# Kernel tuning notes

Measured on AMD Instinct MI355X. Metric: run time of the kernel, lower is better.

The kernel has to match this reference:

```python
import jax, jax.numpy as jnp
import numpy as np

NUM_EMBEDDINGS = 8192
EMBED_DIM = 256
BETA = 0.25  # commitment loss weight (self.beta in the torch module)


def setup_inputs() -> dict:
    key = jax.random.key(0)
    k1, k2 = jax.random.split(key)
    z = jax.random.normal(k1, (16, EMBED_DIM, 32, 32), dtype=jnp.float32)
    # learned codebook (nn.Embedding weight), default init ~ N(0,1); scale for realism
    codebook = jax.random.normal(k2, (NUM_EMBEDDINGS, EMBED_DIM), dtype=jnp.float32)
    return {"z": z, "codebook": codebook}


def reference(z, codebook):
    # channel_last: [B, C, H, W] -> [B, H, W, C]
    zl = jnp.transpose(z, (0, 2, 3, 1))
    # d = ||e||^2 - 2 z.e  (the ||z||^2 term is constant w.r.t. argmin, as in source)
    d = jnp.sum(codebook * codebook, axis=1) - 2.0 * jnp.einsum('bhwd,nd->bhwn', zl, codebook)
    index = jnp.argmin(d, axis=-1)          # [B, H, W] int
    z_q = codebook[index]                   # [B, H, W, C]
    loss = (jnp.mean((jax.lax.stop_gradient(z_q) - zl) ** 2)
            + BETA * jnp.mean((z_q - jax.lax.stop_gradient(zl)) ** 2))
    # straight-through estimator
    z_q_st = zl + jax.lax.stop_gradient(z_q - zl)
    # diversity: mean over batch of (#unique codes used per sample) / (#positions per sample)
    B = index.shape[0]
    flat = index.reshape(B, -1)             # [B, HW]
    presence = jnp.zeros((B, NUM_EMBEDDINGS), jnp.float32).at[
        jnp.arange(B)[:, None], flat].set(1.0)
    diversity = presence.sum() / jnp.float32(flat.size)
    # channel_first: [B, H, W, C] -> [B, C, H, W]
    z_q_out = jnp.transpose(z_q_st, (0, 3, 1, 2))
    return z_q_out, index, loss, diversity
```

## Files before the change

### kernel.cpp

```cpp
#include <hip/hip_runtime.h>
#include <cstdint>

typedef unsigned short u16;
typedef unsigned int   u32;
typedef __attribute__((ext_vector_type(8))) short bf16x8;
typedef __attribute__((ext_vector_type(4))) float f32x4;

#define NPOS    16384
#define DIM     256
#define NCODES  8192
#define ZSTRIDE 262144
#define NELEM   4194304
#define TAU     6e-3f
#define RCH     32


#define WS_AHI    0u
#define WS_ALO    8388608u
#define WS_BHI    16777216u
#define WS_BLO    20971520u
#define WS_E2     25165824u
#define WS_WV1    25198592u
#define WS_WI1    25722880u
#define WS_WV2    26247168u
#define WS_IDX    26771456u
#define WS_PRES   26836992u
#define WS_RCNT   26853376u
#define WS_LDEL   26853380u
#define WS_RLIST  26853632u
#define WS_PART   26919168u
#define WS_RBV    26920448u
#define WS_RBI    29017600u

__device__ __forceinline__ u16 f2bf(float x) {
    u32 u = __float_as_uint(x);
    return (u16)((u + 0x7FFFu + ((u >> 16) & 1u)) >> 16);
}
__device__ __forceinline__ float bf2f(u16 h) { return __uint_as_float((u32)h << 16); }

__device__ __forceinline__ void gload_lds16(const void* g, void* l) {
    __builtin_amdgcn_global_load_lds(
        (const __attribute__((address_space(1))) void*)g,
        (__attribute__((address_space(3))) void*)l, 16, 0, 0);
}

__device__ __forceinline__ void top2_push(float& v1, int& i1, float& v2, float d, int c) {
    const bool better = d < v1;
    v2 = fminf(v2, fmaxf(d, v1));
    v1 = fminf(v1, d);
    if (better) i1 = c;
}
__device__ __forceinline__ void top2_merge(float& v1, int& i1, float& v2,
                                           float ov1, int oi1, float ov2) {
    const bool better = ov1 < v1;
    v2 = fminf(fminf(v2, ov2), fmaxf(v1, ov1));
    v1 = fminf(v1, ov1);
    if (better) i1 = oi1;
}

__global__ __launch_bounds__(256)
void preprocess(const float* __restrict__ cb, const float* __restrict__ z,
                u16* __restrict__ Bhi, u16* __restrict__ Blo,
                u16* __restrict__ Ahi, u16* __restrict__ Alo,
                float* __restrict__ e2, u32* __restrict__ presence,
                int* __restrict__ rcnt, float* __restrict__ ldel) {
    __shared__ u16 his[128 * 34], los[128 * 34];
    const int bid = blockIdx.x;
    const int t   = threadIdx.x;

    if (bid < 2048) {
        if (bid < 16) presence[bid * 256 + t] = 0u;
        if (bid == 16 && t == 0) { rcnt[0] = 0; ldel[0] = 0.0f; }

        const int row  = bid * 4 + (t >> 6);
        const int lane = t & 63;
        const float4 v = *(const float4*)(cb + (size_t)row * DIM + lane * 4);
        float s = v.x * v.x + v.y * v.y + v.z * v.z + v.w * v.w;
#pragma unroll
        for (int o = 32; o > 0; o >>= 1) s += __shfl_xor(s, o);
        if (lane == 0) e2[row] = s;

        const float vv[4] = {v.x, v.y, v.z, v.w};
        u16 h[4], l[4];
#pragma unroll
        for (int j = 0; j < 4; ++j) { h[j] = f2bf(vv[j]); l[j] = f2bf(vv[j] - bf2f(h[j])); }

        const int nt = row >> 7, pr = row & 127, kt = lane >> 3;
        const int q  = (lane & 7) >> 1, off = (lane & 1) * 4;
        const int sw = (pr >> 1) & 3;
        const size_t dst = ((size_t)(nt * 8 + kt) * 128 + pr) * 32 + ((q ^ sw) << 3) + off;
        *(uint2*)(Bhi + dst) = make_uint2((u32)h[0] | ((u32)h[1] << 16), (u32)h[2] | ((u32)h[3] << 16));
        *(uint2*)(Blo + dst) = make_uint2((u32)l[0] | ((u32)l[1] << 16), (u32)l[2] | ((u32)l[3] << 16));
        return;
    }

    const int zb = bid - 2048;
    const int m = zb >> 3, kt = zb & 7;
    const int b = m >> 3, hw0 = (m & 7) * 128;
    const int p = t & 127, ch = t >> 7;

#pragma unroll
    for (int sub = 0; sub < 16; ++sub) {
        const int cl = sub * 2 + ch;
        const float v = z[(size_t)b * ZSTRIDE + (size_t)(kt * 32 + cl) * 1024 + hw0 + p];
        const u16 h = f2bf(v);
        his[p * 34 + cl] = h;
        los[p * 34 + cl] = f2bf(v - bf2f(h));
    }
    __syncthreads();
    const int p2 = t >> 1, c0 = (t & 1) * 2;
    const int sw = (p2 >> 1) & 3;
    const size_t base = ((size_t)(m * 8 + kt) * 128 + p2) * 32;
    u32 wh[8], wl[8];
    const int half = c0 * 8;
#pragma unroll
    for (int j = 0; j < 8; ++j) {
        wh[j] = (u32)his[p2 * 34 + half + 2 * j] | ((u32)his[p2 * 34 + half + 2 * j + 1] << 16);
        wl[j] = (u32)los[p2 * 34 + half + 2 * j] | ((u32)los[p2 * 34 + half + 2 * j + 1] << 16);
    }
    *(uint4*)(Ahi + base + (((c0 + 0) ^ sw) << 3)) = make_uint4(wh[0], wh[1], wh[2], wh[3]);
    *(uint4*)(Ahi + base + (((c0 + 1) ^ sw) << 3)) = make_uint4(wh[4], wh[5], wh[6], wh[7]);
    *(uint4*)(Alo + base + (((c0 + 0) ^ sw) << 3)) = make_uint4(wl[0], wl[1], wl[2], wl[3]);
    *(uint4*)(Alo + base + (((c0 + 1) ^ sw) << 3)) = make_uint4(wl[4], wl[5], wl[6], wl[7]);
}

__global__ __launch_bounds__(256, 2)
void gemm_argmin(const u16* __restrict__ Ahi, const u16* __restrict__ Alo,
                 const u16* __restrict__ Bhi, const u16* __restrict__ Blo,
                 const float* __restrict__ e2,
                 float* __restrict__ wv1, int* __restrict__ wi1, float* __restrict__ wv2) {
    __shared__ u16 sbuf[2][4][4096];
    __shared__ float lv1[256]; __shared__ int li1[256]; __shared__ float lv2[256];

    const int bid = blockIdx.x;
    const int ng  = bid & 7;
    const int mt  = bid >> 3;

    const int tid  = threadIdx.x;
    const int lane = tid & 63;
    const int wvi  = tid >> 6;
    const int wr   = wvi >> 1, wc = wvi & 1;
    const int l15  = lane & 15, lq = lane >> 4;
    const int woff = (tid & 192) * 16;
    const int src  = tid * 8;
    const int sel  = (l15 >> 1) & 3;
    const int ka   = ((lq ^ sel) << 3);

#define FRAG(base, row) (*(const bf16x8*)((base) + (row) * 32 + ka))
#define STAGE(bq, ss_) do {                                                     \
        const int nt_ = ng * 8 + ((ss_) >> 3), kt_ = (ss_) & 7;                 \
        const u16* Ah_ = Ahi + (size_t)(mt * 8 + kt_) * 4096;                   \
        const u16* Al_ = Alo + (size_t)(mt * 8 + kt_) * 4096;                   \
        const u16* Bh_ = Bhi + (size_t)(nt_ * 8 + kt_) * 4096;                  \
        const u16* Bl_ = Blo + (size_t)(nt_ * 8 + kt_) * 4096;                  \
        gload_lds16(Ah_ + src,        (char*)&sbuf[bq][0][0] + woff);           \
        gload_lds16(Ah_ + 2048 + src, (char*)&sbuf[bq][0][0] + 4096 + woff);    \
        gload_lds16(Al_ + src,        (char*)&sbuf[bq][1][0] + woff);           \
        gload_lds16(Al_ + 2048 + src, (char*)&sbuf[bq][1][0] + 4096 + woff);    \
        gload_lds16(Bh_ + src,        (char*)&sbuf[bq][2][0] + woff);           \
        gload_lds16(Bh_ + 2048 + src, (char*)&sbuf[bq][2][0] + 4096 + woff);    \
        gload_lds16(Bl_ + src,        (char*)&sbuf[bq][3][0] + woff);           \
        gload_lds16(Bl_ + 2048 + src, (char*)&sbuf[bq][3][0] + 4096 + woff);    \
    } while (0)

    float rv1[16], rv2[16]; int ri1[16];
#pragma unroll
    for (int e = 0; e < 16; ++e) { rv1[e] = 3e38f; rv2[e] = 3e38f; ri1[e] = 0; }

    f32x4 acc[4][4] = {};
    float e2v[4];
    int cbase = 0;

    STAGE(0, 0);
    __syncthreads();

    for (int ss = 0; ss < 64; ++ss) {
        const int cur = ss & 1;
        if (ss < 63) STAGE(cur ^ 1, ss + 1);

        if ((ss & 7) == 0) {
            const int nt = ng * 8 + (ss >> 3);
            cbase = nt * 128 + wc * 64 + l15;
#pragma unroll
            for (int ni = 0; ni < 4; ++ni) e2v[ni] = e2[cbase + ni * 16];
        }

        const u16* Ah = &sbuf[cur][0][0];
        const u16* Al = &sbuf[cur][1][0];
        const u16* Bh = &sbuf[cur][2][0];
        const u16* Bl = &sbuf[cur][3][0];

        bf16x8 ah[4], bh[4], xx[4];
#pragma unroll
        for (int i = 0; i < 4; ++i) ah[i] = FRAG(Ah, wr * 64 + i * 16 + l15);
#pragma unroll
        for (int i = 0; i < 4; ++i) bh[i] = FRAG(Bh, wc * 64 + i * 16 + l15);
#pragma unroll
        for (int i = 0; i < 4; ++i)
#pragma unroll
            for (int j = 0; j < 4; ++j)
                acc[i][j] = __builtin_amdgcn_mfma_f32_16x16x32_bf16(ah[i], bh[j], acc[i][j], 0, 0, 0);
#pragma unroll
        for (int i = 0; i < 4; ++i) xx[i] = FRAG(Bl, wc * 64 + i * 16 + l15);
#pragma unroll
        for (int i = 0; i < 4; ++i)
#pragma unroll
            for (int j = 0; j < 4; ++j)
                acc[i][j] = __builtin_amdgcn_mfma_f32_16x16x32_bf16(ah[i], xx[j], acc[i][j], 0, 0, 0);
#pragma unroll
        for (int i = 0; i < 4; ++i) xx[i] = FRAG(Al, wr * 64 + i * 16 + l15);
#pragma unroll
        for (int i = 0; i < 4; ++i)
#pragma unroll
            for (int j = 0; j < 4; ++j)
                acc[i][j] = __builtin_amdgcn_mfma_f32_16x16x32_bf16(xx[i], bh[j], acc[i][j], 0, 0, 0);

        if ((ss & 7) == 7) {
#pragma unroll
            for (int mi = 0; mi < 4; ++mi)
#pragma unroll
                for (int j = 0; j < 4; ++j) {
                    const int e = mi * 4 + j;
#pragma unroll
                    for (int ni = 0; ni < 4; ++ni) {
                        const float d = fmaf(-2.0f, acc[mi][ni][j], e2v[ni]);
                        top2_push(rv1[e], ri1[e], rv2[e], d, cbase + ni * 16);
                    }
                }
#pragma unroll
            for (int mi = 0; mi < 4; ++mi)
#pragma unroll
                for (int ni = 0; ni < 4; ++ni)
                    acc[mi][ni] = f32x4{0.f, 0.f, 0.f, 0.f};
        }
        __syncthreads();
    }

#pragma unroll
    for (int mi = 0; mi < 4; ++mi)
#pragma unroll
        for (int j = 0; j < 4; ++j) {
            const int e = mi * 4 + j;
            float v1 = rv1[e], v2 = rv2[e]; int i1 = ri1[e];
#pragma unroll
            for (int off = 1; off <= 8; off <<= 1) {
                const float ov1 = __shfl_xor(v1, off);
                const int   oi1 = __shfl_xor(i1, off);
                const float ov2 = __shfl_xor(v2, off);
                top2_merge(v1, i1, v2, ov1, oi1, ov2);
            }
            if (l15 == 0) {
                const int row = wr * 64 + mi * 16 + lq * 4 + j;
                lv1[row * 2 + wc] = v1; li1[row * 2 + wc] = i1; lv2[row * 2 + wc] = v2;
            }
        }
    __syncthreads();
    if (tid < 128) {
        float v1 = lv1[tid * 2], v2 = lv2[tid * 2]; int i1 = li1[tid * 2];
        top2_merge(v1, i1, v2, lv1[tid * 2 + 1], li1[tid * 2 + 1], lv2[tid * 2 + 1]);
        const size_t o = (size_t)ng * NPOS + (size_t)mt * 128 + tid;
        wv1[o] = v1; wi1[o] = i1; wv2[o] = v2;
    }
#undef FRAG
#undef STAGE
}

__global__ __launch_bounds__(256)
void merge_output(const float* __restrict__ wv1, const int* __restrict__ wi1,
                  const float* __restrict__ wv2,
                  const float* __restrict__ z, const float* __restrict__ cb,
                  float* __restrict__ out, float* __restrict__ out_idxf,
                  float* __restrict__ partial, u32* __restrict__ presence,
                  int* __restrict__ rcnt, int* __restrict__ rlist,
                  int* __restrict__ ws_idx) {
    __shared__ int codes[64];
    __shared__ float red[256];
    const int tile = blockIdx.x;
    const int b    = tile >> 4;
    const int hw0  = (tile & 15) * 64;
    const int tid  = threadIdx.x;
    const int m    = tid & 63;
    const int cg   = tid >> 6;

    if (cg == 0) {
        const int pos = tile * 64 + m;
        float v1 = 3e38f, v2 = 3e38f; int i1 = 0;
#pragma unroll
        for (int g = 0; g < 8; ++g) {
            const size_t o = (size_t)g * NPOS + pos;
            top2_merge(v1, i1, v2, wv1[o], wi1[o], wv2[o]);
        }
        codes[m]      = i1;
        ws_idx[pos]   = i1;
        out_idxf[pos] = (float)i1;
        if (v2 - v1 < TAU) {
            const int s = atomicAdd(rcnt, 1);
            rlist[s] = pos;
        } else {
            atomicOr(&presence[b * 256 + (i1 >> 5)], 1u << (i1 & 31));
        }
    }
    __syncthreads();

    const int code = codes[m];
    const float* crow = cb  + (size_t)code * DIM;
    const float* zb   = z   + (size_t)b * ZSTRIDE + hw0 + m;
    float*       ob   = out + (size_t)b * ZSTRIDE + hw0 + m;

    float lsum = 0.0f;
#pragma unroll
    for (int q = 0; q < 16; ++q) {
        const int c = (cg * 16 + q) * 4;
        const float4 e = *(const float4*)(crow + c);
        const float z0 = zb[(size_t)(c + 0) * 1024];
        const float z1 = zb[(size_t)(c + 1) * 1024];
        const float z2 = zb[(size_t)(c + 2) * 1024];
        const float z3 = zb[(size_t)(c + 3) * 1024];
        const float d0 = e.x - z0, d1 = e.y - z1, d2 = e.z - z2, d3 = e.w - z3;
        lsum += d0 * d0 + d1 * d1 + d2 * d2 + d3 * d3;
        ob[(size_t)(c + 0) * 1024] = z0 + d0;
        ob[(size_t)(c + 1) * 1024] = z1 + d1;
        ob[(size_t)(c + 2) * 1024] = z2 + d2;
        ob[(size_t)(c + 3) * 1024] = z3 + d3;
    }
    red[tid] = lsum;
    __syncthreads();
    for (int o = 128; o > 0; o >>= 1) {
        if (tid < o) red[tid] += red[tid + o];
        __syncthreads();
    }
    if (tid == 0) partial[tile] = red[0];
}

__global__ __launch_bounds__(256)
void rescue_scan(const float* __restrict__ z, const float* __restrict__ cb,
                 const float* __restrict__ e2, const int* __restrict__ rcnt,
                 const int* __restrict__ rlist,
                 float* __restrict__ rbv, int* __restrict__ rbi) {
    __shared__ float zvec[256];
    __shared__ float sv[256]; __shared__ int si[256];
    const int n = rcnt[0];
    const int t = threadIdx.x;
    for (int idx = blockIdx.x; idx < n * RCH; idx += gridDim.x) {
        const int e  = idx >> 5;
        const int ch = idx & 31;
        const int pos = rlist[e];
        const int b = pos >> 10, hw = pos & 1023;
        __syncthreads();
        zvec[t] = z[(size_t)b * ZSTRIDE + (size_t)t * 1024 + hw];
        __syncthreads();

        const int c = ch * 256 + t;
        const float* cr = cb + (size_t)c * DIM;
        float a0 = 0.f, a1 = 0.f, a2 = 0.f, a3 = 0.f;
#pragma unroll
        for (int k = 0; k < DIM; k += 16) {
            const float4 v0 = *(const float4*)(cr + k);
            const float4 v1 = *(const float4*)(cr + k + 4);
            const float4 v2 = *(const float4*)(cr + k + 8);
            const float4 v3 = *(const float4*)(cr + k + 12);
            a0 = fmaf(zvec[k + 0], v0.x, a0); a0 = fmaf(zvec[k + 1], v0.y, a0);
            a0 = fmaf(zvec[k + 2], v0.z, a0); a0 = fmaf(zvec[k + 3], v0.w, a0);
            a1 = fmaf(zvec[k + 4], v1.x, a1); a1 = fmaf(zvec[k + 5], v1.y, a1);
            a1 = fmaf(zvec[k + 6], v1.z, a1); a1 = fmaf(zvec[k + 7], v1.w, a1);
            a2 = fmaf(zvec[k + 8], v2.x, a2); a2 = fmaf(zvec[k + 9], v2.y, a2);
            a2 = fmaf(zvec[k +10], v2.z, a2); a2 = fmaf(zvec[k +11], v2.w, a2);
            a3 = fmaf(zvec[k +12], v3.x, a3); a3 = fmaf(zvec[k +13], v3.y, a3);
            a3 = fmaf(zvec[k +14], v3.z, a3); a3 = fmaf(zvec[k +15], v3.w, a3);
        }
        const float dot = (a0 + a1) + (a2 + a3);
        sv[t] = fmaf(-2.f, dot, e2[c]); si[t] = c;
        __syncthreads();
        for (int o = 128; o > 0; o >>= 1) {
            if (t < o) {
                const float ov = sv[t + o]; const int oi = si[t + o];
                if (ov < sv[t] || (ov == sv[t] && oi < si[t])) { sv[t] = ov; si[t] = oi; }
            }
            __syncthreads();
        }
        if (t == 0) { rbv[e * RCH + ch] = sv[0]; rbi[e * RCH + ch] = si[0]; }
    }
}

__global__ __launch_bounds__(256)
void rescue_fix(const float* __restrict__ z, const float* __restrict__ cb,
                const int* __restrict__ rcnt, const int* __restrict__ rlist,
                const float* __restrict__ rbv, const int* __restrict__ rbi,
                const int* __restrict__ ws_idx,
                float* __restrict__ out_idxf, u32* __restrict__ presence,
                float* __restrict__ out, float* __restrict__ ldel) {
    __shared__ int   bestc;
    __shared__ float red[4];
    const int n = rcnt[0];
    const int t = threadIdx.x;
    for (int e = blockIdx.x; e < n; e += gridDim.x) {
        const int pos = rlist[e];
        const int b = pos >> 10, hw = pos & 1023;
        if (t == 0) {
            float bv = 3e38f; int bi = 0x7fffffff;
            for (int ch = 0; ch < RCH; ++ch) {
                const float v = rbv[e * RCH + ch]; const int i = rbi[e * RCH + ch];
                if (v < bv || (v == bv && i < bi)) { bv = v; bi = i; }
            }
            bestc = bi;
            out_idxf[pos] = (float)bi;
            atomicOr(&presence[b * 256 + (bi >> 5)], 1u << (bi & 31));
        }
        __syncthreads();
        const int best = bestc;
        const int old  = ws_idx[pos];
        if (best != old) {
            const float zv = z[(size_t)b * ZSTRIDE + (size_t)t * 1024 + hw];
            const float en = cb[(size_t)best * DIM + t];
            const float eo = cb[(size_t)old  * DIM + t];
            const float dn = en - zv, dold = eo - zv;
            out[(size_t)b * ZSTRIDE + (size_t)t * 1024 + hw] = zv + dn;
            float dl = dn * dn - dold * dold;
#pragma unroll
            for (int o = 32; o > 0; o >>= 1) dl += __shfl_xor(dl, o);
            if ((t & 63) == 0) red[t >> 6] = dl;
            __syncthreads();
            if (t == 0) atomicAdd(ldel, red[0] + red[1] + red[2] + red[3]);
        }
        __syncthreads();
    }
}

__global__ __launch_bounds__(256)
void finalize_kernel(const float* __restrict__ partial,
                     const u32* __restrict__ presence,
                     const float* __restrict__ ldel,
                     float* __restrict__ out_loss, float* __restrict__ out_div) {
    __shared__ float sred[256];
    __shared__ int   ired[256];
    const int tid = threadIdx.x;
    float s = partial[tid];
    int cnt = 0;
    for (int w = tid; w < 16 * 256; w += 256) cnt += __popc(presence[w]);
    sred[tid] = s; ired[tid] = cnt;
    __syncthreads();
    for (int o = 128; o > 0; o >>= 1) {
        if (tid < o) { sred[tid] += sred[tid + o]; ired[tid] += ired[tid + o]; }
        __syncthreads();
    }
    if (tid == 0) {
        out_loss[0] = 1.25f * (sred[0] + ldel[0]) / (float)NELEM;
        out_div[0]  = (float)ired[0] / (float)NPOS;
    }
}

extern "C" void kernel_launch(void* const* d_in, const int* in_sizes, int n_in,
                              void* d_out, int out_size, void* d_ws, size_t ws_size,
                              hipStream_t stream) {
    const float* z  = (const float*)d_in[0];
    const float* cb = (const float*)d_in[1];
    float* out = (float*)d_out;
    char*  ws  = (char*)d_ws;

    u16*   Ahi = (u16*)(ws + WS_AHI);
    u16*   Alo = (u16*)(ws + WS_ALO);
    u16*   Bhi = (u16*)(ws + WS_BHI);
    u16*   Blo = (u16*)(ws + WS_BLO);
    float* e2  = (float*)(ws + WS_E2);
    float* wv1 = (float*)(ws + WS_WV1);
    int*   wi1 = (int*)(ws + WS_WI1);
    float* wv2 = (float*)(ws + WS_WV2);
    int*   ws_idx = (int*)(ws + WS_IDX);
    u32*   presence = (u32*)(ws + WS_PRES);
    int*   rcnt  = (int*)(ws + WS_RCNT);
    float* ldel  = (float*)(ws + WS_LDEL);
    int*   rlist = (int*)(ws + WS_RLIST);
    float* partial = (float*)(ws + WS_PART);
    float* rbv = (float*)(ws + WS_RBV);
    int*   rbi = (int*)(ws + WS_RBI);

    float* out_zq   = out;
    float* out_idxf = out + NELEM;
    float* out_loss = out + NELEM + NPOS;
    float* out_div  = out + NELEM + NPOS + 1;

    preprocess<<<3072, 256, 0, stream>>>(cb, z, Bhi, Blo, Ahi, Alo, e2, presence, rcnt, ldel);
    gemm_argmin<<<1024, 256, 0, stream>>>(Ahi, Alo, Bhi, Blo, e2, wv1, wi1, wv2);
    merge_output<<<NPOS / 64, 256, 0, stream>>>(wv1, wi1, wv2, z, cb, out_zq, out_idxf,
                                                partial, presence, rcnt, rlist, ws_idx);
    rescue_scan<<<2048, 256, 0, stream>>>(z, cb, e2, rcnt, rlist, rbv, rbi);
    rescue_fix<<<256, 256, 0, stream>>>(z, cb, rcnt, rlist, rbv, rbi, ws_idx,
                                        out_idxf, presence, out_zq, ldel);
    finalize_kernel<<<1, 256, 0, stream>>>(partial, presence, ldel, out_loss, out_div);
}
```

Measured before the change: 256.5 us.

## Cache e2 in LDS, relax GEMM barriers, warp-level reductions in rescue kernels

The GEMM kernel now copies its slice of codebook norms into shared memory once per block. Its per-step __syncthreads is replaced by an explicit vmcnt wait plus a raw s_barrier, so the prefetch of the next stage can stay in flight while the current one is consumed. The rescue scan gives each wave four codes per thread and reduces with wave shuffles instead of an LDS tree reduction with many block barriers. The rescue fix merges its 32 chunk results with a wave shuffle and launches more blocks. The hand-written waitcnt depends on the exact count of outstanding loads and could cause races if the compiler schedules differently.

```diff
diff --git a/kernel.cpp b/kernel.cpp
--- a/kernel.cpp
+++ b/kernel.cpp
@@ -130,6 +130,7 @@
                  const float* __restrict__ e2,
                  float* __restrict__ wv1, int* __restrict__ wi1, float* __restrict__ wv2) {
     __shared__ u16 sbuf[2][4][4096];
+    __shared__ __align__(16) float e2s[1024];
     __shared__ float lv1[256]; __shared__ int li1[256]; __shared__ float lv2[256];
 
     const int bid = blockIdx.x;
@@ -171,18 +172,27 @@
     float e2v[4];
     int cbase = 0;
 
+    reinterpret_cast<float4*>(e2s)[tid] = ((const float4*)e2)[ng * 256 + tid];
+    __syncthreads();
     STAGE(0, 0);
-    __syncthreads();
 
     for (int ss = 0; ss < 64; ++ss) {
         const int cur = ss & 1;
-        if (ss < 63) STAGE(cur ^ 1, ss + 1);
+        if (ss < 63) {
+            STAGE(cur ^ 1, ss + 1);
+            asm volatile("s_waitcnt vmcnt(8)" ::: "memory");
+        } else {
+            asm volatile("s_waitcnt vmcnt(0)" ::: "memory");
+        }
+        __builtin_amdgcn_s_barrier();
+        __builtin_amdgcn_sched_barrier(0);
 
         if ((ss & 7) == 0) {
-            const int nt = ng * 8 + (ss >> 3);
-            cbase = nt * 128 + wc * 64 + l15;
-#pragma unroll
-            for (int ni = 0; ni < 4; ++ni) e2v[ni] = e2[cbase + ni * 16];
+            const int ntl = ss >> 3;
+            cbase = (ng * 8 + ntl) * 128 + wc * 64 + l15;
+            const int eb = ntl * 128 + wc * 64 + l15;
+#pragma unroll
+            for (int ni = 0; ni < 4; ++ni) e2v[ni] = e2s[eb + ni * 16];
         }
 
         const u16* Ah = &sbuf[cur][0][0];
@@ -233,7 +243,7 @@
                 for (int ni = 0; ni < 4; ++ni)
                     acc[mi][ni] = f32x4{0.f, 0.f, 0.f, 0.f};
         }
-        __syncthreads();
+        __builtin_amdgcn_s_barrier();
     }
 
 #pragma unroll
@@ -338,47 +348,53 @@
                  const int* __restrict__ rlist,
                  float* __restrict__ rbv, int* __restrict__ rbi) {
     __shared__ float zvec[256];
-    __shared__ float sv[256]; __shared__ int si[256];
     const int n = rcnt[0];
     const int t = threadIdx.x;
-    for (int idx = blockIdx.x; idx < n * RCH; idx += gridDim.x) {
-        const int e  = idx >> 5;
-        const int ch = idx & 31;
+    const int w = t >> 6, l = t & 63;
+    const int njobs = n * 8;
+    for (int idx = blockIdx.x; idx < njobs; idx += gridDim.x) {
+        const int e  = idx >> 3;
+        const int cg = idx & 7;
         const int pos = rlist[e];
         const int b = pos >> 10, hw = pos & 1023;
         __syncthreads();
         zvec[t] = z[(size_t)b * ZSTRIDE + (size_t)t * 1024 + hw];
         __syncthreads();
 
-        const int c = ch * 256 + t;
-        const float* cr = cb + (size_t)c * DIM;
-        float a0 = 0.f, a1 = 0.f, a2 = 0.f, a3 = 0.f;
-#pragma unroll
-        for (int k = 0; k < DIM; k += 16) {
-            const float4 v0 = *(const float4*)(cr + k);
-            const float4 v1 = *(const float4*)(cr + k + 4);
-            const float4 v2 = *(const float4*)(cr + k + 8);
-            const float4 v3 = *(const float4*)(cr + k + 12);
-            a0 = fmaf(zvec[k + 0], v0.x, a0); a0 = fmaf(zvec[k + 1], v0.y, a0);
-            a0 = fmaf(zvec[k + 2], v0.z, a0); a0 = fmaf(zvec[k + 3], v0.w, a0);
-            a1 = fmaf(zvec[k + 4], v1.x, a1); a1 = fmaf(zvec[k + 5], v1.y, a1);
-            a1 = fmaf(zvec[k + 6], v1.z, a1); a1 = fmaf(zvec[k + 7], v1.w, a1);
-            a2 = fmaf(zvec[k + 8], v2.x, a2); a2 = fmaf(zvec[k + 9], v2.y, a2);
-            a2 = fmaf(zvec[k +10], v2.z, a2); a2 = fmaf(zvec[k +11], v2.w, a2);
-            a3 = fmaf(zvec[k +12], v3.x, a3); a3 = fmaf(zvec[k +13], v3.y, a3);
-            a3 = fmaf(zvec[k +14], v3.z, a3); a3 = fmaf(zvec[k +15], v3.w, a3);
-        }
-        const float dot = (a0 + a1) + (a2 + a3);
-        sv[t] = fmaf(-2.f, dot, e2[c]); si[t] = c;
-        __syncthreads();
-        for (int o = 128; o > 0; o >>= 1) {
-            if (t < o) {
-                const float ov = sv[t + o]; const int oi = si[t + o];
-                if (ov < sv[t] || (ov == sv[t] && oi < si[t])) { sv[t] = ov; si[t] = oi; }
+        const int ch = cg * 4 + w;
+        const int c0 = ch * 256 + l * 4;
+        float bv = 3e38f; int bi = 0x7fffffff;
+#pragma unroll
+        for (int j = 0; j < 4; ++j) {
+            const int c = c0 + j;
+            const float* cr = cb + (size_t)c * DIM;
+            float a0 = 0.f, a1 = 0.f, a2 = 0.f, a3 = 0.f;
+#pragma unroll
+            for (int k = 0; k < DIM; k += 16) {
+                const float4 v0 = *(const float4*)(cr + k);
+                const float4 v1 = *(const float4*)(cr + k + 4);
+                const float4 v2 = *(const float4*)(cr + k + 8);
+                const float4 v3 = *(const float4*)(cr + k + 12);
+                a0 = fmaf(zvec[k + 0], v0.x, a0); a0 = fmaf(zvec[k + 1], v0.y, a0);
+                a0 = fmaf(zvec[k + 2], v0.z, a0); a0 = fmaf(zvec[k + 3], v0.w, a0);
+                a1 = fmaf(zvec[k + 4], v1.x, a1); a1 = fmaf(zvec[k + 5], v1.y, a1);
+                a1 = fmaf(zvec[k + 6], v1.z, a1); a1 = fmaf(zvec[k + 7], v1.w, a1);
+                a2 = fmaf(zvec[k + 8], v2.x, a2); a2 = fmaf(zvec[k + 9], v2.y, a2);
+                a2 = fmaf(zvec[k +10], v2.z, a2); a2 = fmaf(zvec[k +11], v2.w, a2);
+                a3 = fmaf(zvec[k +12], v3.x, a3); a3 = fmaf(zvec[k +13], v3.y, a3);
+                a3 = fmaf(zvec[k +14], v3.z, a3); a3 = fmaf(zvec[k +15], v3.w, a3);
             }
-            __syncthreads();
-        }
-        if (t == 0) { rbv[e * RCH + ch] = sv[0]; rbi[e * RCH + ch] = si[0]; }
+            const float dot = (a0 + a1) + (a2 + a3);
+            const float d = fmaf(-2.f, dot, e2[c]);
+            if (d < bv) { bv = d; bi = c; }
+        }
+#pragma unroll
+        for (int off = 1; off <= 32; off <<= 1) {
+            const float ov = __shfl_xor(bv, off);
+            const int   oi = __shfl_xor(bi, off);
+            if (ov < bv || (ov == bv && oi < bi)) { bv = ov; bi = oi; }
+        }
+        if (l == 0) { rbv[e * RCH + ch] = bv; rbi[e * RCH + ch] = bi; }
     }
 }
 
@@ -389,25 +405,30 @@
                 const int* __restrict__ ws_idx,
                 float* __restrict__ out_idxf, u32* __restrict__ presence,
                 float* __restrict__ out, float* __restrict__ ldel) {
-    __shared__ int   bestc;
+    __shared__ int   bestc_sh;
     __shared__ float red[4];
     const int n = rcnt[0];
     const int t = threadIdx.x;
     for (int e = blockIdx.x; e < n; e += gridDim.x) {
         const int pos = rlist[e];
         const int b = pos >> 10, hw = pos & 1023;
-        if (t == 0) {
-            float bv = 3e38f; int bi = 0x7fffffff;
-            for (int ch = 0; ch < RCH; ++ch) {
-                const float v = rbv[e * RCH + ch]; const int i = rbi[e * RCH + ch];
-                if (v < bv || (v == bv && i < bi)) { bv = v; bi = i; }
+        if (t < 64) {
+            float v = 3e38f; int i = 0x7fffffff;
+            if (t < 32) { v = rbv[e * RCH + t]; i = rbi[e * RCH + t]; }
+#pragma unroll
+            for (int off = 1; off <= 32; off <<= 1) {
+                const float ov = __shfl_xor(v, off);
+                const int   oi = __shfl_xor(i, off);
+                if (ov < v || (ov == v && oi < i)) { v = ov; i = oi; }
             }
-            bestc = bi;
-            out_idxf[pos] = (float)bi;
-            atomicOr(&presence[b * 256 + (bi >> 5)], 1u << (bi & 31));
+            if (t == 0) {
+                bestc_sh = i;
+                out_idxf[pos] = (float)i;
+                atomicOr(&presence[b * 256 + (i >> 5)], 1u << (i & 31));
+            }
         }
         __syncthreads();
-        const int best = bestc;
+        const int best = bestc_sh;
         const int old  = ws_idx[pos];
         if (best != old) {
             const float zv = z[(size_t)b * ZSTRIDE + (size_t)t * 1024 + hw];
@@ -484,7 +505,7 @@
     merge_output<<<NPOS / 64, 256, 0, stream>>>(wv1, wi1, wv2, z, cb, out_zq, out_idxf,
                                                 partial, presence, rcnt, rlist, ws_idx);
     rescue_scan<<<2048, 256, 0, stream>>>(z, cb, e2, rcnt, rlist, rbv, rbi);
-    rescue_fix<<<256, 256, 0, stream>>>(z, cb, rcnt, rlist, rbv, rbi, ws_idx,
+    rescue_fix<<<512, 256, 0, stream>>>(z, cb, rcnt, rlist, rbv, rbi, ws_idx,
                                         out_idxf, presence, out_zq, ldel);
     finalize_kernel<<<1, 256, 0, stream>>>(partial, presence, ldel, out_loss, out_div);
 }
```

Measured after the change: 263.6 us. 1.03x slower.
